# Performance work log

Measured on AMD Instinct MI355X. Metric: run time of the kernel, lower is better.

Reference implementation:

```python
import jax, jax.numpy as jnp
import numpy as np

EMBED_DIM = 768
NUM_HEADS = 12
HEAD_DIM = EMBED_DIM // NUM_HEADS


def setup_inputs() -> dict:
    key = jax.random.key(0)
    ks = jax.random.split(key, 9)
    B, N, D = 8, 1024, EMBED_DIM
    s = 1.0 / np.sqrt(D)
    x = jax.random.normal(ks[0], (B, N, D), dtype=jnp.float32)
    Wq = jax.random.normal(ks[1], (D, D), dtype=jnp.float32) * s
    bq = jnp.zeros((D,), dtype=jnp.float32)
    Wk = jax.random.normal(ks[2], (D, D), dtype=jnp.float32) * s
    bk = jnp.zeros((D,), dtype=jnp.float32)
    Wv = jax.random.normal(ks[3], (D, D), dtype=jnp.float32) * s
    bv = jnp.zeros((D,), dtype=jnp.float32)
    Wo = jax.random.normal(ks[4], (D, D), dtype=jnp.float32) * s
    bo = jnp.zeros((D,), dtype=jnp.float32)
    return {"x": x, "Wq": Wq, "bq": bq, "Wk": Wk, "bk": bk,
            "Wv": Wv, "bv": bv, "Wo": Wo, "bo": bo}


def reference(x, Wq, bq, Wk, bk, Wv, bv, Wo, bo):
    B, N, D = x.shape
    H, Hd = NUM_HEADS, HEAD_DIM
    # torch Linear: y = x @ W.T + b
    q = (x @ Wq.T + bq).reshape(B, N, H, Hd).transpose(0, 2, 1, 3)  # [B,H,N,Hd]
    k = (x @ Wk.T + bk).reshape(B, N, H, Hd).transpose(0, 2, 1, 3)
    v = (x @ Wv.T + bv).reshape(B, N, H, Hd).transpose(0, 2, 1, 3)
    # NOTE: original scales by embed_dim**-0.5 (not head_dim)
    scale = jnp.asarray(D, x.dtype) ** -0.5
    scores = jnp.einsum('bhnd,bhmd->bhnm', q, k) * scale  # [B,H,N,N]
    attn = jax.nn.softmax(scores, axis=-1)
    out = jnp.einsum('bhnm,bhmd->bhnd', attn, v)  # dropout: identity in eval
    out = out.transpose(0, 2, 1, 3).reshape(B, N, D)
    return out @ Wo.T + bo
```

## Files before the change

kernel.cpp:

```cpp
#include <hip/hip_runtime.h>
#include <math.h>


typedef __bf16 bf16x8 __attribute__((ext_vector_type(8)));
typedef float  f32x4  __attribute__((ext_vector_type(4)));
typedef unsigned u32x2 __attribute__((ext_vector_type(2)));
typedef unsigned u32x4 __attribute__((ext_vector_type(4)));
typedef unsigned short ushort_t;

__device__ __forceinline__ unsigned short f2bf(float f) {
    unsigned u = __float_as_uint(f);
    u += 0x7fffu + ((u >> 16) & 1u);
    return (unsigned short)(u >> 16);
}
__device__ __forceinline__ unsigned pk16(unsigned short lo, unsigned short hi) {
    return (unsigned)lo | ((unsigned)hi << 16);
}

#define GLL16(g, l)                                                                        \
    __builtin_amdgcn_global_load_lds((const __attribute__((address_space(1))) void*)(g),   \
                                     (__attribute__((address_space(3))) void*)(l), 16, 0, 0)

__global__ __launch_bounds__(256)
void cast_all(const float* __restrict__ x,
              const float* __restrict__ w0, const float* __restrict__ w1,
              const float* __restrict__ w2, const float* __restrict__ w3,
              ushort_t* __restrict__ xb, ushort_t* __restrict__ wb0,
              ushort_t* __restrict__ wb1, ushort_t* __restrict__ wb2,
              ushort_t* __restrict__ wb3)
{
    const int y = blockIdx.y;
    if (y == 0) {
        const int i = (blockIdx.x * 256 + threadIdx.x) * 8;
        const float4 f0 = *(const float4*)(x + i);
        const float4 f1 = *(const float4*)(x + i + 4);
        ushort4 p0, p1;
        p0.x = f2bf(f0.x); p0.y = f2bf(f0.y); p0.z = f2bf(f0.z); p0.w = f2bf(f0.w);
        p1.x = f2bf(f1.x); p1.y = f2bf(f1.y); p1.z = f2bf(f1.z); p1.w = f2bf(f1.w);
        *(ushort4*)(xb + i)     = p0;
        *(ushort4*)(xb + i + 4) = p1;
        return;
    }
    const int tile = blockIdx.x * 4 + (threadIdx.x >> 6);
    if (tile >= 48 * 24) return;
    const float* s; ushort_t* d;
    switch (y) {
        case 1:  s = w0; d = wb0; break;
        case 2:  s = w1; d = wb1; break;
        case 3:  s = w2; d = wb2; break;
        default: s = w3; d = wb3; break;
    }
    const int t = tile / 24, kb = tile % 24;
    const int L = threadIdx.x & 63, c = L & 15, g = L >> 4;
    const float* sp = s + (size_t)(t * 16 + c) * 768 + kb * 32 + g * 8;
    const float4 f0 = *(const float4*)sp;
    const float4 f1 = *(const float4*)(sp + 4);
    ushort4 p0, p1;
    p0.x = f2bf(f0.x); p0.y = f2bf(f0.y); p0.z = f2bf(f0.z); p0.w = f2bf(f0.w);
    p1.x = f2bf(f1.x); p1.y = f2bf(f1.y); p1.z = f2bf(f1.z); p1.w = f2bf(f1.w);
    ushort_t* dp = d + ((size_t)tile * 64 + L) * 8;
    *(ushort4*)dp       = p0;
    *(ushort4*)(dp + 4) = p1;
}

__global__ __launch_bounds__(256, 3)
void gemm_qkv(const ushort_t* __restrict__ xb,
              const ushort_t* __restrict__ wqb, const ushort_t* __restrict__ wkb,
              const ushort_t* __restrict__ wvb,
              const float* __restrict__ bq, const float* __restrict__ bk,
              const float* __restrict__ bv,
              ushort_t* __restrict__ Qh, ushort_t* __restrict__ Kl,
              ushort_t* __restrict__ Vl)
{
    __shared__ ushort_t smem[9216];
    ushort_t* As = smem;

    const int tid = threadIdx.x, L = tid & 63, wv = tid >> 6;
    const int c = L & 15, g = L >> 4;
    const int n0 = blockIdx.x * 128, m0 = blockIdx.y * 64;

    const int qs = ((tid & 3) ^ ((tid >> 3) & 3)) * 8;
    const ushort_t* ap = xb + (size_t)(m0 + (tid >> 2)) * 768 + qs;
    const int sg = (g ^ ((c >> 1) & 3)) * 8;

    const size_t wbase = ((size_t)(blockIdx.x * 8 + wv * 2) * 24 * 64 + L) * 8;
    const ushort_t* wqp = wqb + wbase;
    const ushort_t* wkp = wkb + wbase;
    const ushort_t* wvp = wvb + wbase;

    f32x4 acc[3][4][2];
#pragma unroll
    for (int z = 0; z < 3; ++z)
#pragma unroll
        for (int i = 0; i < 4; ++i)
#pragma unroll
            for (int j = 0; j < 2; ++j) acc[z][i][j] = (f32x4){0.f, 0.f, 0.f, 0.f};

    bf16x8 wf[3][2];
#pragma unroll
    for (int j = 0; j < 2; ++j) {
        wf[0][j] = *(const bf16x8*)(wqp + j * 12288);
        wf[1][j] = *(const bf16x8*)(wkp + j * 12288);
        wf[2][j] = *(const bf16x8*)(wvp + j * 12288);
    }

    for (int kb = 0; kb < 24; ++kb) {
        __syncthreads();
        GLL16(ap + kb * 32, &As[(size_t)tid * 8]);
        __syncthreads();
        bf16x8 af[4];
#pragma unroll
        for (int i = 0; i < 4; ++i)
            af[i] = *(const bf16x8*)&As[(i * 16 + c) * 32 + sg];
#pragma unroll
        for (int z = 0; z < 3; ++z)
#pragma unroll
            for (int i = 0; i < 4; ++i)
#pragma unroll
                for (int j = 0; j < 2; ++j)
                    acc[z][i][j] = __builtin_amdgcn_mfma_f32_16x16x32_bf16(
                        af[i], wf[z][j], acc[z][i][j], 0, 0, 0);
        const int kn = (kb < 23) ? kb + 1 : 23;
#pragma unroll
        for (int j = 0; j < 2; ++j) {
            wf[0][j] = *(const bf16x8*)(wqp + j * 12288 + kn * 512);
            wf[1][j] = *(const bf16x8*)(wkp + j * 12288 + kn * 512);
            wf[2][j] = *(const bf16x8*)(wvp + j * 12288 + kn * 512);
        }
    }

    const int b  = m0 >> 10, nb = m0 & 1023;
    const int hcol = n0 + wv * 32;
    const int h = hcol >> 6, uh = (hcol >> 5) & 1;
    const int bh = b * 12 + h;
    ushort_t* scr = smem + wv * 2304;

    float bias2[3][2];
#pragma unroll
    for (int j = 0; j < 2; ++j) {
        bias2[0][j] = bq[hcol + j * 16 + c];
        bias2[1][j] = bk[hcol + j * 16 + c];
        bias2[2][j] = bv[hcol + j * 16 + c];
    }

    __syncthreads();

#pragma unroll
    for (int i = 0; i < 4; ++i)
#pragma unroll
        for (int j = 0; j < 2; ++j)
#pragma unroll
            for (int r = 0; r < 4; ++r)
                scr[(i * 16 + g * 4 + r) * 36 + j * 16 + c] =
                    f2bf(acc[0][i][j][r] + bias2[0][j]);
#pragma unroll
    for (int e = 0; e < 4; ++e) {
        const int slot = e * 64 + L;
        const int row = slot >> 2, ch = slot & 3;
        const u32x4 v = *(const u32x4*)&scr[row * 36 + ch * 8];
        *(u32x4*)&Qh[((size_t)bh * 1024 + nb + row) * 64 + uh * 32 + ch * 8] = v;
    }

#pragma unroll
    for (int i = 0; i < 4; ++i)
#pragma unroll
        for (int j = 0; j < 2; ++j)
#pragma unroll
            for (int r = 0; r < 4; ++r)
                scr[(i * 16 + g * 4 + r) * 36 + j * 16 + c] =
                    f2bf(acc[1][i][j][r] + bias2[1][j]);
#pragma unroll
    for (int tau = 0; tau < 4; ++tau) {
        const u32x4 v = *(const u32x4*)&scr[(tau * 16 + c) * 36 + g * 8];
        *(u32x4*)&Kl[(((size_t)bh * 64 + (nb >> 4) + tau) * 2 + uh) * 512
                     + (size_t)L * 8] = v;
    }

#pragma unroll
    for (int i = 0; i < 4; ++i)
#pragma unroll
        for (int j = 0; j < 2; ++j)
#pragma unroll
            for (int r = 0; r < 4; ++r)
                scr[(j * 16 + c) * 68 + i * 16 + g * 4 + r] =
                    f2bf(acc[2][i][j][r] + bias2[2][j]);
    const int T = nb >> 6;
#pragma unroll
    for (int t = 0; t < 4; ++t) {
        const int htl = t >> 1, u = t & 1;
        const u32x4 v = *(const u32x4*)&scr[(htl * 16 + c) * 68 + u * 32 + g * 8];
        *(u32x4*)&Vl[((((size_t)bh * 4 + uh * 2 + htl) * 16 + T) * 2 + u) * 512
                     + (size_t)L * 8] = v;
    }
}

__global__ __launch_bounds__(256, 3)
void gemm_outp(const ushort_t* __restrict__ attnb, const ushort_t* __restrict__ wob,
               const float* __restrict__ bo, float* __restrict__ out)
{
    __shared__ ushort_t smem[2048];
    ushort_t* As = smem;
    const int tid = threadIdx.x, L = tid & 63, wv = tid >> 6;
    const int c = L & 15, g = L >> 4;
    const int n0 = blockIdx.x * 128, m0 = blockIdx.y * 64;
    const int qs = ((tid & 3) ^ ((tid >> 3) & 3)) * 8;
    const ushort_t* ap = attnb + (size_t)(m0 + (tid >> 2)) * 768 + qs;
    const int sg = (g ^ ((c >> 1) & 3)) * 8;

    const size_t wbase = ((size_t)(blockIdx.x * 8 + wv * 2) * 24 * 64 + L) * 8;
    const ushort_t* wop = wob + wbase;

    f32x4 acc[4][2];
#pragma unroll
    for (int i = 0; i < 4; ++i)
#pragma unroll
        for (int j = 0; j < 2; ++j) acc[i][j] = (f32x4){0.f, 0.f, 0.f, 0.f};

    bf16x8 wf[2];
#pragma unroll
    for (int j = 0; j < 2; ++j) wf[j] = *(const bf16x8*)(wop + j * 12288);

    for (int kb = 0; kb < 24; ++kb) {
        __syncthreads();
        GLL16(ap + kb * 32, &As[(size_t)tid * 8]);
        __syncthreads();
        bf16x8 af[4];
#pragma unroll
        for (int i = 0; i < 4; ++i)
            af[i] = *(const bf16x8*)&As[(i * 16 + c) * 32 + sg];
#pragma unroll
        for (int i = 0; i < 4; ++i)
#pragma unroll
            for (int j = 0; j < 2; ++j)
                acc[i][j] = __builtin_amdgcn_mfma_f32_16x16x32_bf16(
                    af[i], wf[j], acc[i][j], 0, 0, 0);
        const int kn = (kb < 23) ? kb + 1 : 23;
#pragma unroll
        for (int j = 0; j < 2; ++j)
            wf[j] = *(const bf16x8*)(wop + j * 12288 + kn * 512);
    }

#pragma unroll
    for (int i = 0; i < 4; ++i) {
        const int row = m0 + i * 16 + g * 4;
#pragma unroll
        for (int j = 0; j < 2; ++j) {
            const int col = n0 + wv * 32 + j * 16 + c;
            const float bsvo = bo[col];
#pragma unroll
            for (int r = 0; r < 4; ++r)
                out[(size_t)(row + r) * 768 + col] = acc[i][j][r] + bsvo;
        }
    }
}

__global__ __launch_bounds__(64, 3)
void flash_bf16(const ushort_t* __restrict__ Q, const ushort_t* __restrict__ Kl,
                const ushort_t* __restrict__ Vl, ushort_t* __restrict__ attnb)
{
    __shared__ ushort_t Ps[2][2][16 * 68];
    const int L = threadIdx.x;
    const int c = L & 15, g = L >> 4;
    const int bh = blockIdx.x, q0 = blockIdx.y * 32;
    const float SC2 = 0.05205954985329743f;

    const ushort_t* Qp = Q + ((size_t)bh * 1024 + q0 + c) * 64 + g * 8;
    bf16x8 qf[2][2];
    qf[0][0] = *(const bf16x8*)Qp;
    qf[0][1] = *(const bf16x8*)(Qp + 32);
    qf[1][0] = *(const bf16x8*)(Qp + 16 * 64);
    qf[1][1] = *(const bf16x8*)(Qp + 16 * 64 + 32);

    const ushort_t* Kb = Kl + (size_t)bh * 65536 + (size_t)L * 8;
    const ushort_t* Vb = Vl + (size_t)bh * 65536 + (size_t)L * 8;

    f32x4 o[2][4];
#pragma unroll
    for (int w = 0; w < 2; ++w)
#pragma unroll
        for (int ht = 0; ht < 4; ++ht) o[w][ht] = (f32x4){0.f, 0.f, 0.f, 0.f};
    float ls[2] = {0.f, 0.f};

    bf16x8 kf0[4], kf1[4];
#pragma unroll
    for (int ct = 0; ct < 4; ++ct) {
        kf0[ct] = *(const bf16x8*)(Kb + (size_t)(ct * 2 + 0) * 512);
        kf1[ct] = *(const bf16x8*)(Kb + (size_t)(ct * 2 + 1) * 512);
    }

    for (int T0 = 0; T0 < 16; T0 += 2) {
#pragma unroll
        for (int p = 0; p < 2; ++p) {
            const int T = T0 + p;
            bf16x8 vf0[4], vf1[4];
#pragma unroll
            for (int ht = 0; ht < 4; ++ht) {
                const ushort_t* vp = Vb + (size_t)((ht * 16 + T) * 2) * 512;
                vf0[ht] = *(const bf16x8*)vp;
                vf1[ht] = *(const bf16x8*)(vp + 512);
            }
            f32x4 s[2][4];
#pragma unroll
            for (int w = 0; w < 2; ++w)
#pragma unroll
                for (int ct = 0; ct < 4; ++ct) {
                    f32x4 zz = (f32x4){0.f, 0.f, 0.f, 0.f};
                    zz = __builtin_amdgcn_mfma_f32_16x16x32_bf16(kf0[ct], qf[w][0], zz, 0, 0, 0);
                    zz = __builtin_amdgcn_mfma_f32_16x16x32_bf16(kf1[ct], qf[w][1], zz, 0, 0, 0);
                    s[w][ct] = zz;
                }
            const int Tn = (T < 15) ? T + 1 : 15;
#pragma unroll
            for (int ct = 0; ct < 4; ++ct) {
                const ushort_t* kp = Kb + (size_t)((Tn * 4 + ct) * 2) * 512;
                kf0[ct] = *(const bf16x8*)kp;
                kf1[ct] = *(const bf16x8*)(kp + 512);
            }
#pragma unroll
            for (int w = 0; w < 2; ++w) {
#pragma unroll
                for (int ct = 0; ct < 4; ++ct) {
                    float pv[4];
#pragma unroll
                    for (int r = 0; r < 4; ++r)
                        pv[r] = __builtin_amdgcn_exp2f(s[w][ct][r] * SC2);
                    ls[w] += (pv[0] + pv[1]) + (pv[2] + pv[3]);
                    const unsigned w01 = __builtin_amdgcn_perm(
                        __float_as_uint(pv[1]), __float_as_uint(pv[0]), 0x07060302u);
                    const unsigned w23 = __builtin_amdgcn_perm(
                        __float_as_uint(pv[3]), __float_as_uint(pv[2]), 0x07060302u);
                    *(u32x2*)&Ps[p][w][c * 68 + ct * 16 + g * 4] = (u32x2){w01, w23};
                }
            }
#pragma unroll
            for (int w = 0; w < 2; ++w) {
                const int pb = c * 68 + g * 8;
                const u32x4 pa  = *(const u32x4*)&Ps[p][w][pb];
                const u32x4 pbv = *(const u32x4*)&Ps[p][w][pb + 32];
                const bf16x8 pf0 = __builtin_bit_cast(bf16x8, pa);
                const bf16x8 pf1 = __builtin_bit_cast(bf16x8, pbv);
#pragma unroll
                for (int ht = 0; ht < 4; ++ht) {
                    o[w][ht] = __builtin_amdgcn_mfma_f32_16x16x32_bf16(vf0[ht], pf0, o[w][ht], 0, 0, 0);
                    o[w][ht] = __builtin_amdgcn_mfma_f32_16x16x32_bf16(vf1[ht], pf1, o[w][ht], 0, 0, 0);
                }
            }
        }
    }

    const int b = bh / 12, h = bh % 12;
#pragma unroll
    for (int w = 0; w < 2; ++w) {
        float l = ls[w];
        l += __shfl_xor(l, 16);
        l += __shfl_xor(l, 32);
        const float inv = 1.f / l;
#pragma unroll
        for (int ht = 0; ht < 4; ++ht) {
            const unsigned w0 = pk16(f2bf(o[w][ht][0] * inv), f2bf(o[w][ht][1] * inv));
            const unsigned w1 = pk16(f2bf(o[w][ht][2] * inv), f2bf(o[w][ht][3] * inv));
            *(u32x2*)&Ps[0][w][c * 68 + ht * 16 + g * 4] = (u32x2){w0, w1};
        }
#pragma unroll
        for (int e = 0; e < 2; ++e) {
            const int row = e * 8 + (L >> 3);
            const int ch  = L & 7;
            const int si  = row * 68 + ch * 8;
            const u32x2 t0 = *(const u32x2*)&Ps[0][w][si];
            const u32x2 t1 = *(const u32x2*)&Ps[0][w][si + 4];
            *(u32x4*)&attnb[((size_t)(b * 1024 + q0 + w * 16 + row)) * 768 + h * 64 + ch * 8]
                = (u32x4){t0.x, t0.y, t1.x, t1.y};
        }
    }
}

extern "C" void kernel_launch(void* const* d_in, const int* in_sizes, int n_in,
                              void* d_out, int out_size, void* d_ws, size_t ws_size,
                              hipStream_t stream)
{
    const float* x  = (const float*)d_in[0];
    const float* Wq = (const float*)d_in[1];
    const float* bq = (const float*)d_in[2];
    const float* Wk = (const float*)d_in[3];
    const float* bk = (const float*)d_in[4];
    const float* Wv = (const float*)d_in[5];
    const float* bv = (const float*)d_in[6];
    const float* Wo = (const float*)d_in[7];
    const float* bo = (const float*)d_in[8];
    float* out = (float*)d_out;

    char* ws = (char*)d_ws;
    ushort_t* xb    = (ushort_t*)(ws);
    ushort_t* wqb   = (ushort_t*)(ws + 12582912);
    ushort_t* wkb   = (ushort_t*)(ws + 12582912 + 1179648);
    ushort_t* wvb   = (ushort_t*)(ws + 12582912 + 2359296);
    ushort_t* wob   = (ushort_t*)(ws + 12582912 + 3538944);
    ushort_t* Qh    = (ushort_t*)(ws + 17301504);
    ushort_t* Kl    = (ushort_t*)(ws + 29884416);
    ushort_t* Vl    = (ushort_t*)(ws + 42467328);
    ushort_t* attnb = (ushort_t*)(ws + 55050240);

    cast_all<<<dim3(3072, 5), 256, 0, stream>>>(x, Wq, Wk, Wv, Wo,
                                                xb, wqb, wkb, wvb, wob);
    gemm_qkv<<<dim3(6, 128), 256, 0, stream>>>(xb, wqb, wkb, wvb,
                                               bq, bk, bv, Qh, Kl, Vl);
    flash_bf16<<<dim3(96, 32), 64, 0, stream>>>(Qh, Kl, Vl, attnb);
    gemm_outp<<<dim3(6, 128), 256, 0, stream>>>(attnb, wob, bo, out);
}
```

Baseline: 191.2 us.

## Split flash attention into four waves per block, one 16-row query tile each

Before, each 64-thread block handled 32 query rows. Now each 256-thread block holds four wavefronts, and each wave handles 16 query rows. Per-wave register use falls (one query tile, half the accumulators), which allows more waves in flight per CU. K/V are still loaded per wave from global memory, so the waves in a block share them only through cache. The change adds a __syncthreads per two-tile step, which waves do not need since each uses its own shared-memory slot.

```diff
diff --git a/kernel.cpp b/kernel.cpp
--- a/kernel.cpp
+++ b/kernel.cpp
@@ -254,32 +254,29 @@
     }
 }
 
-__global__ __launch_bounds__(64, 3)
+__global__ __launch_bounds__(256, 6)
 void flash_bf16(const ushort_t* __restrict__ Q, const ushort_t* __restrict__ Kl,
                 const ushort_t* __restrict__ Vl, ushort_t* __restrict__ attnb)
 {
-    __shared__ ushort_t Ps[2][2][16 * 68];
-    const int L = threadIdx.x;
+    __shared__ ushort_t Ps[2][4][16 * 68];
+    const int tid = threadIdx.x;
+    const int L = tid & 63, w = tid >> 6;
     const int c = L & 15, g = L >> 4;
-    const int bh = blockIdx.x, q0 = blockIdx.y * 32;
+    const int bh = blockIdx.x, q0 = blockIdx.y * 64 + w * 16;
     const float SC2 = 0.05205954985329743f;
 
     const ushort_t* Qp = Q + ((size_t)bh * 1024 + q0 + c) * 64 + g * 8;
-    bf16x8 qf[2][2];
-    qf[0][0] = *(const bf16x8*)Qp;
-    qf[0][1] = *(const bf16x8*)(Qp + 32);
-    qf[1][0] = *(const bf16x8*)(Qp + 16 * 64);
-    qf[1][1] = *(const bf16x8*)(Qp + 16 * 64 + 32);
+    bf16x8 qf[2];
+    qf[0] = *(const bf16x8*)Qp;
+    qf[1] = *(const bf16x8*)(Qp + 32);
 
     const ushort_t* Kb = Kl + (size_t)bh * 65536 + (size_t)L * 8;
     const ushort_t* Vb = Vl + (size_t)bh * 65536 + (size_t)L * 8;
 
-    f32x4 o[2][4];
-#pragma unroll
-    for (int w = 0; w < 2; ++w)
-#pragma unroll
-        for (int ht = 0; ht < 4; ++ht) o[w][ht] = (f32x4){0.f, 0.f, 0.f, 0.f};
-    float ls[2] = {0.f, 0.f};
+    f32x4 o[4];
+#pragma unroll
+    for (int ht = 0; ht < 4; ++ht) o[ht] = (f32x4){0.f, 0.f, 0.f, 0.f};
+    float ls = 0.f;
 
     bf16x8 kf0[4], kf1[4];
 #pragma unroll
@@ -289,6 +286,7 @@
     }
 
     for (int T0 = 0; T0 < 16; T0 += 2) {
+        __syncthreads();
 #pragma unroll
         for (int p = 0; p < 2; ++p) {
             const int T = T0 + p;
@@ -299,16 +297,14 @@
                 vf0[ht] = *(const bf16x8*)vp;
                 vf1[ht] = *(const bf16x8*)(vp + 512);
             }
-            f32x4 s[2][4];
-#pragma unroll
-            for (int w = 0; w < 2; ++w)
-#pragma unroll
-                for (int ct = 0; ct < 4; ++ct) {
-                    f32x4 zz = (f32x4){0.f, 0.f, 0.f, 0.f};
-                    zz = __builtin_amdgcn_mfma_f32_16x16x32_bf16(kf0[ct], qf[w][0], zz, 0, 0, 0);
-                    zz = __builtin_amdgcn_mfma_f32_16x16x32_bf16(kf1[ct], qf[w][1], zz, 0, 0, 0);
-                    s[w][ct] = zz;
-                }
+            f32x4 s[4];
+#pragma unroll
+            for (int ct = 0; ct < 4; ++ct) {
+                f32x4 zz = (f32x4){0.f, 0.f, 0.f, 0.f};
+                zz = __builtin_amdgcn_mfma_f32_16x16x32_bf16(kf0[ct], qf[0], zz, 0, 0, 0);
+                zz = __builtin_amdgcn_mfma_f32_16x16x32_bf16(kf1[ct], qf[1], zz, 0, 0, 0);
+                s[ct] = zz;
+            }
             const int Tn = (T < 15) ? T + 1 : 15;
 #pragma unroll
             for (int ct = 0; ct < 4; ++ct) {
@@ -317,23 +313,19 @@
                 kf1[ct] = *(const bf16x8*)(kp + 512);
             }
 #pragma unroll
-            for (int w = 0; w < 2; ++w) {
-#pragma unroll
-                for (int ct = 0; ct < 4; ++ct) {
-                    float pv[4];
-#pragma unroll
-                    for (int r = 0; r < 4; ++r)
-                        pv[r] = __builtin_amdgcn_exp2f(s[w][ct][r] * SC2);
-                    ls[w] += (pv[0] + pv[1]) + (pv[2] + pv[3]);
-                    const unsigned w01 = __builtin_amdgcn_perm(
-                        __float_as_uint(pv[1]), __float_as_uint(pv[0]), 0x07060302u);
-                    const unsigned w23 = __builtin_amdgcn_perm(
-                        __float_as_uint(pv[3]), __float_as_uint(pv[2]), 0x07060302u);
-                    *(u32x2*)&Ps[p][w][c * 68 + ct * 16 + g * 4] = (u32x2){w01, w23};
-                }
+            for (int ct = 0; ct < 4; ++ct) {
+                float pv[4];
+#pragma unroll
+                for (int r = 0; r < 4; ++r)
+                    pv[r] = __builtin_amdgcn_exp2f(s[ct][r] * SC2);
+                ls += (pv[0] + pv[1]) + (pv[2] + pv[3]);
+                const unsigned w01 = __builtin_amdgcn_perm(
+                    __float_as_uint(pv[1]), __float_as_uint(pv[0]), 0x07060302u);
+                const unsigned w23 = __builtin_amdgcn_perm(
+                    __float_as_uint(pv[3]), __float_as_uint(pv[2]), 0x07060302u);
+                *(u32x2*)&Ps[p][w][c * 68 + ct * 16 + g * 4] = (u32x2){w01, w23};
             }
-#pragma unroll
-            for (int w = 0; w < 2; ++w) {
+            {
                 const int pb = c * 68 + g * 8;
                 const u32x4 pa  = *(const u32x4*)&Ps[p][w][pb];
                 const u32x4 pbv = *(const u32x4*)&Ps[p][w][pb + 32];
@@ -341,24 +333,23 @@
                 const bf16x8 pf1 = __builtin_bit_cast(bf16x8, pbv);
 #pragma unroll
                 for (int ht = 0; ht < 4; ++ht) {
-                    o[w][ht] = __builtin_amdgcn_mfma_f32_16x16x32_bf16(vf0[ht], pf0, o[w][ht], 0, 0, 0);
-                    o[w][ht] = __builtin_amdgcn_mfma_f32_16x16x32_bf16(vf1[ht], pf1, o[w][ht], 0, 0, 0);
+                    o[ht] = __builtin_amdgcn_mfma_f32_16x16x32_bf16(vf0[ht], pf0, o[ht], 0, 0, 0);
+                    o[ht] = __builtin_amdgcn_mfma_f32_16x16x32_bf16(vf1[ht], pf1, o[ht], 0, 0, 0);
                 }
             }
         }
     }
 
     const int b = bh / 12, h = bh % 12;
-#pragma unroll
-    for (int w = 0; w < 2; ++w) {
-        float l = ls[w];
+    {
+        float l = ls;
         l += __shfl_xor(l, 16);
         l += __shfl_xor(l, 32);
         const float inv = 1.f / l;
 #pragma unroll
         for (int ht = 0; ht < 4; ++ht) {
-            const unsigned w0 = pk16(f2bf(o[w][ht][0] * inv), f2bf(o[w][ht][1] * inv));
-            const unsigned w1 = pk16(f2bf(o[w][ht][2] * inv), f2bf(o[w][ht][3] * inv));
+            const unsigned w0 = pk16(f2bf(o[ht][0] * inv), f2bf(o[ht][1] * inv));
+            const unsigned w1 = pk16(f2bf(o[ht][2] * inv), f2bf(o[ht][3] * inv));
             *(u32x2*)&Ps[0][w][c * 68 + ht * 16 + g * 4] = (u32x2){w0, w1};
         }
 #pragma unroll
@@ -368,7 +359,7 @@
             const int si  = row * 68 + ch * 8;
             const u32x2 t0 = *(const u32x2*)&Ps[0][w][si];
             const u32x2 t1 = *(const u32x2*)&Ps[0][w][si + 4];
-            *(u32x4*)&attnb[((size_t)(b * 1024 + q0 + w * 16 + row)) * 768 + h * 64 + ch * 8]
+            *(u32x4*)&attnb[((size_t)(b * 1024 + q0 + row)) * 768 + h * 64 + ch * 8]
                 = (u32x4){t0.x, t0.y, t1.x, t1.y};
         }
     }
@@ -404,6 +395,6 @@
                                                 xb, wqb, wkb, wvb, wob);
     gemm_qkv<<<dim3(6, 128), 256, 0, stream>>>(xb, wqb, wkb, wvb,
                                                bq, bk, bv, Qh, Kl, Vl);
-    flash_bf16<<<dim3(96, 32), 64, 0, stream>>>(Qh, Kl, Vl, attnb);
+    flash_bf16<<<dim3(96, 16), 256, 0, stream>>>(Qh, Kl, Vl, attnb);
     gemm_outp<<<dim3(6, 128), 256, 0, stream>>>(attnb, wob, bo, out);
 }
```

New measurement: 238.6 us. 24.7% more time.

## Split flash attention key range across two waves with LDS reduction

Applied to the files above, without the earlier changes.

The flash kernel now launches two wavefronts per block. Each wave processes half of the key/value tiles for the same 32 query rows, and the partial outputs and row sums are combined through shared memory at the end. This doubles the number of waves available to hide latency without adding blocks, at the cost of a cross-wave reduction, two barriers and more shared memory. Softmax still uses no max subtraction, so the unnormalized partials can simply be added.

```diff
diff --git a/kernel.cpp b/kernel.cpp
--- a/kernel.cpp
+++ b/kernel.cpp
@@ -254,12 +254,13 @@
     }
 }
 
-__global__ __launch_bounds__(64, 3)
+__global__ __launch_bounds__(128, 5)
 void flash_bf16(const ushort_t* __restrict__ Q, const ushort_t* __restrict__ Kl,
                 const ushort_t* __restrict__ Vl, ushort_t* __restrict__ attnb)
 {
-    __shared__ ushort_t Ps[2][2][16 * 68];
-    const int L = threadIdx.x;
+    __shared__ ushort_t smem[6528];
+    const int tid = threadIdx.x;
+    const int L = tid & 63, w = tid >> 6;
     const int c = L & 15, g = L >> 4;
     const int bh = blockIdx.x, q0 = blockIdx.y * 32;
     const float SC2 = 0.05205954985329743f;
@@ -274,103 +275,123 @@
     const ushort_t* Kb = Kl + (size_t)bh * 65536 + (size_t)L * 8;
     const ushort_t* Vb = Vl + (size_t)bh * 65536 + (size_t)L * 8;
 
+    ushort_t* st0 = smem + (w * 2 + 0) * 1088;
+    ushort_t* st1 = smem + (w * 2 + 1) * 1088;
+
     f32x4 o[2][4];
 #pragma unroll
-    for (int w = 0; w < 2; ++w)
-#pragma unroll
-        for (int ht = 0; ht < 4; ++ht) o[w][ht] = (f32x4){0.f, 0.f, 0.f, 0.f};
+    for (int u = 0; u < 2; ++u)
+#pragma unroll
+        for (int ht = 0; ht < 4; ++ht) o[u][ht] = (f32x4){0.f, 0.f, 0.f, 0.f};
     float ls[2] = {0.f, 0.f};
 
+    const int Tbeg = w * 8;
     bf16x8 kf0[4], kf1[4];
 #pragma unroll
     for (int ct = 0; ct < 4; ++ct) {
-        kf0[ct] = *(const bf16x8*)(Kb + (size_t)(ct * 2 + 0) * 512);
-        kf1[ct] = *(const bf16x8*)(Kb + (size_t)(ct * 2 + 1) * 512);
-    }
-
-    for (int T0 = 0; T0 < 16; T0 += 2) {
-#pragma unroll
-        for (int p = 0; p < 2; ++p) {
-            const int T = T0 + p;
-            bf16x8 vf0[4], vf1[4];
+        const ushort_t* kp = Kb + (size_t)((Tbeg * 4 + ct) * 2) * 512;
+        kf0[ct] = *(const bf16x8*)kp;
+        kf1[ct] = *(const bf16x8*)(kp + 512);
+    }
+
+#pragma unroll 2
+    for (int T = Tbeg; T < Tbeg + 8; ++T) {
+        bf16x8 vf0[4], vf1[4];
+#pragma unroll
+        for (int ht = 0; ht < 4; ++ht) {
+            const ushort_t* vp = Vb + (size_t)((ht * 16 + T) * 2) * 512;
+            vf0[ht] = *(const bf16x8*)vp;
+            vf1[ht] = *(const bf16x8*)(vp + 512);
+        }
+        f32x4 s[2][4];
+#pragma unroll
+        for (int u = 0; u < 2; ++u)
+#pragma unroll
+            for (int ct = 0; ct < 4; ++ct) {
+                f32x4 zz = (f32x4){0.f, 0.f, 0.f, 0.f};
+                zz = __builtin_amdgcn_mfma_f32_16x16x32_bf16(kf0[ct], qf[u][0], zz, 0, 0, 0);
+                zz = __builtin_amdgcn_mfma_f32_16x16x32_bf16(kf1[ct], qf[u][1], zz, 0, 0, 0);
+                s[u][ct] = zz;
+            }
+        const int Tn = (T < Tbeg + 7) ? T + 1 : T;
+#pragma unroll
+        for (int ct = 0; ct < 4; ++ct) {
+            const ushort_t* kp = Kb + (size_t)((Tn * 4 + ct) * 2) * 512;
+            kf0[ct] = *(const bf16x8*)kp;
+            kf1[ct] = *(const bf16x8*)(kp + 512);
+        }
+#pragma unroll
+        for (int u = 0; u < 2; ++u) {
+            ushort_t* st = u ? st1 : st0;
+#pragma unroll
+            for (int ct = 0; ct < 4; ++ct) {
+                float pv[4];
+#pragma unroll
+                for (int r = 0; r < 4; ++r)
+                    pv[r] = __builtin_amdgcn_exp2f(s[u][ct][r] * SC2);
+                ls[u] += (pv[0] + pv[1]) + (pv[2] + pv[3]);
+                const unsigned w01 = __builtin_amdgcn_perm(
+                    __float_as_uint(pv[1]), __float_as_uint(pv[0]), 0x07060302u);
+                const unsigned w23 = __builtin_amdgcn_perm(
+                    __float_as_uint(pv[3]), __float_as_uint(pv[2]), 0x07060302u);
+                *(u32x2*)&st[c * 68 + ct * 16 + g * 4] = (u32x2){w01, w23};
+            }
+        }
+#pragma unroll
+        for (int u = 0; u < 2; ++u) {
+            const ushort_t* st = u ? st1 : st0;
+            const int pb = c * 68 + g * 8;
+            const u32x4 pa  = *(const u32x4*)&st[pb];
+            const u32x4 pbv = *(const u32x4*)&st[pb + 32];
+            const bf16x8 pf0 = __builtin_bit_cast(bf16x8, pa);
+            const bf16x8 pf1 = __builtin_bit_cast(bf16x8, pbv);
 #pragma unroll
             for (int ht = 0; ht < 4; ++ht) {
-                const ushort_t* vp = Vb + (size_t)((ht * 16 + T) * 2) * 512;
-                vf0[ht] = *(const bf16x8*)vp;
-                vf1[ht] = *(const bf16x8*)(vp + 512);
+                o[u][ht] = __builtin_amdgcn_mfma_f32_16x16x32_bf16(vf0[ht], pf0, o[u][ht], 0, 0, 0);
+                o[u][ht] = __builtin_amdgcn_mfma_f32_16x16x32_bf16(vf1[ht], pf1, o[u][ht], 0, 0, 0);
             }
-            f32x4 s[2][4];
-#pragma unroll
-            for (int w = 0; w < 2; ++w)
-#pragma unroll
-                for (int ct = 0; ct < 4; ++ct) {
-                    f32x4 zz = (f32x4){0.f, 0.f, 0.f, 0.f};
-                    zz = __builtin_amdgcn_mfma_f32_16x16x32_bf16(kf0[ct], qf[w][0], zz, 0, 0, 0);
-                    zz = __builtin_amdgcn_mfma_f32_16x16x32_bf16(kf1[ct], qf[w][1], zz, 0, 0, 0);
-                    s[w][ct] = zz;
-                }
-            const int Tn = (T < 15) ? T + 1 : 15;
-#pragma unroll
-            for (int ct = 0; ct < 4; ++ct) {
-                const ushort_t* kp = Kb + (size_t)((Tn * 4 + ct) * 2) * 512;
-                kf0[ct] = *(const bf16x8*)kp;
-                kf1[ct] = *(const bf16x8*)(kp + 512);
-            }
-#pragma unroll
-            for (int w = 0; w < 2; ++w) {
-#pragma unroll
-                for (int ct = 0; ct < 4; ++ct) {
-                    float pv[4];
-#pragma unroll
-                    for (int r = 0; r < 4; ++r)
-                        pv[r] = __builtin_amdgcn_exp2f(s[w][ct][r] * SC2);
-                    ls[w] += (pv[0] + pv[1]) + (pv[2] + pv[3]);
-                    const unsigned w01 = __builtin_amdgcn_perm(
-                        __float_as_uint(pv[1]), __float_as_uint(pv[0]), 0x07060302u);
-                    const unsigned w23 = __builtin_amdgcn_perm(
-                        __float_as_uint(pv[3]), __float_as_uint(pv[2]), 0x07060302u);
-                    *(u32x2*)&Ps[p][w][c * 68 + ct * 16 + g * 4] = (u32x2){w01, w23};
-                }
-            }
-#pragma unroll
-            for (int w = 0; w < 2; ++w) {
-                const int pb = c * 68 + g * 8;
-                const u32x4 pa  = *(const u32x4*)&Ps[p][w][pb];
-                const u32x4 pbv = *(const u32x4*)&Ps[p][w][pb + 32];
-                const bf16x8 pf0 = __builtin_bit_cast(bf16x8, pa);
-                const bf16x8 pf1 = __builtin_bit_cast(bf16x8, pbv);
-#pragma unroll
-                for (int ht = 0; ht < 4; ++ht) {
-                    o[w][ht] = __builtin_amdgcn_mfma_f32_16x16x32_bf16(vf0[ht], pf0, o[w][ht], 0, 0, 0);
-                    o[w][ht] = __builtin_amdgcn_mfma_f32_16x16x32_bf16(vf1[ht], pf1, o[w][ht], 0, 0, 0);
-                }
-            }
         }
     }
 
     const int b = bh / 12, h = bh % 12;
-#pragma unroll
-    for (int w = 0; w < 2; ++w) {
-        float l = ls[w];
-        l += __shfl_xor(l, 16);
-        l += __shfl_xor(l, 32);
-        const float inv = 1.f / l;
-#pragma unroll
-        for (int ht = 0; ht < 4; ++ht) {
-            const unsigned w0 = pk16(f2bf(o[w][ht][0] * inv), f2bf(o[w][ht][1] * inv));
-            const unsigned w1 = pk16(f2bf(o[w][ht][2] * inv), f2bf(o[w][ht][3] * inv));
-            *(u32x2*)&Ps[0][w][c * 68 + ht * 16 + g * 4] = (u32x2){w0, w1};
-        }
-#pragma unroll
-        for (int e = 0; e < 2; ++e) {
-            const int row = e * 8 + (L >> 3);
-            const int ch  = L & 7;
-            const int si  = row * 68 + ch * 8;
-            const u32x2 t0 = *(const u32x2*)&Ps[0][w][si];
-            const u32x2 t1 = *(const u32x2*)&Ps[0][w][si + 4];
-            *(u32x4*)&attnb[((size_t)(b * 1024 + q0 + w * 16 + row)) * 768 + h * 64 + ch * 8]
-                = (u32x4){t0.x, t0.y, t1.x, t1.y};
-        }
+    float* oF  = (float*)smem;
+    float* lsF = oF + 2048;
+    const int uo = 1 - w;
+
+    __syncthreads();
+#pragma unroll
+    for (int ht = 0; ht < 4; ++ht)
+#pragma unroll
+        for (int r = 0; r < 4; ++r)
+            oF[w * 1024 + (ht * 4 + r) * 64 + L] = o[uo][ht][r];
+    lsF[w * 64 + L] = ls[uo];
+    __syncthreads();
+
+    float l = ls[w] + lsF[uo * 64 + L];
+    l += __shfl_xor(l, 16);
+    l += __shfl_xor(l, 32);
+    const float inv = 1.f / l;
+
+    ushort_t* strip = smem + 4352 + w * 1088;
+#pragma unroll
+    for (int ht = 0; ht < 4; ++ht) {
+        const float v0 = o[w][ht][0] + oF[uo * 1024 + (ht * 4 + 0) * 64 + L];
+        const float v1 = o[w][ht][1] + oF[uo * 1024 + (ht * 4 + 1) * 64 + L];
+        const float v2 = o[w][ht][2] + oF[uo * 1024 + (ht * 4 + 2) * 64 + L];
+        const float v3 = o[w][ht][3] + oF[uo * 1024 + (ht * 4 + 3) * 64 + L];
+        const unsigned w0 = pk16(f2bf(v0 * inv), f2bf(v1 * inv));
+        const unsigned w1 = pk16(f2bf(v2 * inv), f2bf(v3 * inv));
+        *(u32x2*)&strip[c * 68 + ht * 16 + g * 4] = (u32x2){w0, w1};
+    }
+#pragma unroll
+    for (int e = 0; e < 2; ++e) {
+        const int row = e * 8 + (L >> 3);
+        const int ch  = L & 7;
+        const int si  = row * 68 + ch * 8;
+        const u32x2 t0 = *(const u32x2*)&strip[si];
+        const u32x2 t1 = *(const u32x2*)&strip[si + 4];
+        *(u32x4*)&attnb[((size_t)(b * 1024 + q0 + w * 16 + row)) * 768 + h * 64 + ch * 8]
+            = (u32x4){t0.x, t0.y, t1.x, t1.y};
     }
 }
 
@@ -404,6 +425,6 @@
                                                 xb, wqb, wkb, wvb, wob);
     gemm_qkv<<<dim3(6, 128), 256, 0, stream>>>(xb, wqb, wkb, wvb,
                                                bq, bk, bv, Qh, Kl, Vl);
-    flash_bf16<<<dim3(96, 32), 64, 0, stream>>>(Qh, Kl, Vl, attnb);
+    flash_bf16<<<dim3(96, 32), 128, 0, stream>>>(Qh, Kl, Vl, attnb);
     gemm_outp<<<dim3(6, 128), 256, 0, stream>>>(attnb, wob, bo, out);
 }
```

Measured after the change: 439.0 us. 130% more time.
